# Kernel optimization log

Hardware: AMD Instinct MI355X
Metric: run time of the kernel (lower is better)

The kernel has to match this reference:

```python
import jax, jax.numpy as jnp
import numpy as np

POOL_NUM = 1024
NEIGHBOR_NUM = 16


def setup_inputs() -> dict:
    key = jax.random.key(0)
    k1, k2 = jax.random.split(key)
    vertices = jax.random.normal(k1, (8, 4096, 3), dtype=jnp.float32)
    feature_map = jax.random.normal(k2, (8, 4096, 256), dtype=jnp.float32)
    return {"vertices": vertices, "feature_map": feature_map}


def _get_neighbor_index(vertices, neighbor_num):
    # vertices: (bs, N, 3) -> neighbor_index: (bs, N, neighbor_num)
    inner = jnp.einsum('bnd,bmd->bnm', vertices, vertices)  # (bs, N, N)
    quadratic = jnp.sum(vertices ** 2, axis=2)              # (bs, N)
    distance = -2.0 * inner + quadratic[:, None, :] + quadratic[:, :, None]
    # smallest k+1 distances -> top_k on negated distance
    _, idx = jax.lax.top_k(-distance, neighbor_num + 1)     # (bs, N, k+1)
    return idx[:, :, 1:]                                    # drop self


def reference(vertices, feature_map):
    bs, vertice_num, _ = vertices.shape
    neighbor_index = _get_neighbor_index(vertices, NEIGHBOR_NUM)  # (bs, N, k)
    # gather neighbor features: (bs, N, k, C)
    id_0 = jnp.arange(bs)[:, None, None]
    neighbor_feature = feature_map[id_0, neighbor_index]
    pooled_feature = jnp.max(neighbor_feature, axis=2)            # (bs, N, C)
    # deterministic random subsample of vertices (torch uses randperm)
    sample_idx = jax.random.permutation(jax.random.key(42), vertice_num)[:POOL_NUM]
    vertices_pool = vertices[:, sample_idx, :]                    # (bs, P, 3)
    feature_map_pool = pooled_feature[:, sample_idx, :]           # (bs, P, C)
    return (vertices_pool, feature_map_pool)
```

## Files before the change

### kernel.cpp

```cpp
#include <hip/hip_runtime.h>
#include <stdint.h>
#include <string.h>
#include <algorithm>

#define NV 4096
#define NPOOL 1024
#define NB 8
#define KNB 16
#define REMOVED 0xFFFFFFFFu
#define HIDX(b) ((((b) >> 4) | (((b) & 15) << 6)))

struct SIdx { unsigned short v[NPOOL]; };

static inline void tf2x32_host(uint32_t k0, uint32_t k1,
                               uint32_t c0, uint32_t c1,
                               uint32_t& o0, uint32_t& o1) {
  uint32_t ks0 = k0, ks1 = k1, ks2 = k0 ^ k1 ^ 0x1BD11BDAu;
  uint32_t x0 = c0 + ks0, x1 = c1 + ks1;
#define TFR(r) { x0 += x1; x1 = (x1 << (r)) | (x1 >> (32 - (r))); x1 ^= x0; }
  TFR(13) TFR(15) TFR(26) TFR(6)
  x0 += ks1; x1 += ks2 + 1u;
  TFR(17) TFR(29) TFR(16) TFR(24)
  x0 += ks2; x1 += ks0 + 2u;
  TFR(13) TFR(15) TFR(26) TFR(6)
  x0 += ks0; x1 += ks1 + 3u;
  TFR(17) TFR(29) TFR(16) TFR(24)
  x0 += ks1; x1 += ks2 + 4u;
  TFR(13) TFR(15) TFR(26) TFR(6)
  x0 += ks2; x1 += ks0 + 5u;
#undef TFR
  o0 = x0; o1 = x1;
}

static void compute_sample_idx(SIdx& out) {
  static_assert(sizeof(SIdx) == 2048, "kernarg size");
  uint64_t arr[NV];
  uint16_t x[NV], tmp[NV];
  for (int i = 0; i < NV; ++i) x[i] = (uint16_t)i;
  uint32_t kh = 0u, kl = 42u;
  for (int round = 0; round < 2; ++round) {
    uint32_t nkh, nkl, sh, sl, t0, t1;
    tf2x32_host(kh, kl, 0u, 0u, nkh, nkl);
    tf2x32_host(kh, kl, 0u, 1u, sh, sl);
    kh = nkh; kl = nkl;
    for (int i = 0; i < NV; ++i) {
      tf2x32_host(sh, sl, 0u, (uint32_t)i, t0, t1);
      arr[i] = ((uint64_t)(t0 ^ t1) << 32) | (uint32_t)i;
    }
    std::sort(arr, arr + NV);
    for (int i = 0; i < NV; ++i) tmp[i] = x[(uint32_t)(arr[i] & 0xffffffffu)];
    memcpy(x, tmp, sizeof(x));
  }
  for (int i = 0; i < NPOOL; ++i) out.v[i] = x[i];
}

#define FALLBACK(D, TAUB, WIN)                                             \
  {                                                                        \
    uint32_t mask = 0;                                                     \
    for (int r = 0; r < KNB; ++r) {                                        \
      uint32_t bv = REMOVED, bm = 0xFFFFFFFFu;                             \
      _Pragma("unroll")                                                    \
      for (int t = 0; t < 16; ++t) {                                       \
        const uint32_t v = (((mask >> t) & 1u) || ((D[t] >> 22) > (TAUB))) \
                               ? REMOVED : D[t];                           \
        const uint32_t m = (uint32_t)((tid << 4) + t);                     \
        if (v < bv || (v == bv && m < bm)) { bv = v; bm = m; }             \
      }                                                                    \
      for (int off = 32; off > 0; off >>= 1) {                             \
        const uint32_t ov = (uint32_t)__shfl_down((int)bv, off);           \
        const uint32_t om = (uint32_t)__shfl_down((int)bm, off);           \
        if (ov < bv || (ov == bv && om < bm)) { bv = ov; bm = om; }        \
      }                                                                    \
      if (lane == 0) wmin[warp] = ((unsigned long long)bv << 32) | bm;     \
      __syncthreads();                                                     \
      const unsigned long long p0 = wmin[0], p1 = wmin[1];                 \
      const unsigned long long p2 = wmin[2], p3 = wmin[3];                 \
      const unsigned long long pa = (p0 < p1) ? p0 : p1;                   \
      const unsigned long long pb = (p2 < p3) ? p2 : p3;                   \
      const int w = (int)(((pa < pb) ? pa : pb) & 0xFFFFFFFFu);            \
      if (tid == 0) (WIN)[r] = w;                                          \
      if (tid == (w >> 4)) mask |= 1u << (w & 15);                         \
      __syncthreads();                                                     \
    }                                                                      \
  }

__global__ __launch_bounds__(256) void knn_pool_kernel(
    const float* __restrict__ vertices, const float* __restrict__ fm,
    const SIdx sidx,
    float* __restrict__ outV, float* __restrict__ outF) {
  __shared__ uint32_t hist0[1024], hist1[1024];
  __shared__ unsigned long long cand0[64], cand1[64];
  __shared__ unsigned long long wmin[4];
  __shared__ int winners0[KNB], winners1[KNB];
  __shared__ int s_nc0, s_nc1, s_tb0, s_tb1;

  const int tid = threadIdx.x;
  const int lane = tid & 63;
  const int warp = tid >> 6;
  const int blk = blockIdx.x;
  const int b = blk & 7;
  const int i0 = (blk >> 3) << 1;
  const int i1 = i0 | 1;
  const int n0 = (int)sidx.v[i0];
  const int n1 = (int)sidx.v[i1];

  const float* vb = vertices + (size_t)b * NV * 3;
  const float q0x = vb[n0 * 3 + 0], q0y = vb[n0 * 3 + 1], q0z = vb[n0 * 3 + 2];
  const float q1x = vb[n1 * 3 + 0], q1y = vb[n1 * 3 + 1], q1z = vb[n1 * 3 + 2];
  const float qn0 = __fadd_rn(__fadd_rn(__fmul_rn(q0x, q0x), __fmul_rn(q0y, q0y)),
                              __fmul_rn(q0z, q0z));
  const float qn1 = __fadd_rn(__fadd_rn(__fmul_rn(q1x, q1x), __fmul_rn(q1y, q1y)),
                              __fmul_rn(q1z, q1z));

  const float4* vb4 = (const float4*)vb + tid * 12;
  float f[48];
#pragma unroll
  for (int j = 0; j < 12; ++j) {
    const float4 v4 = vb4[j];
    f[4 * j + 0] = v4.x; f[4 * j + 1] = v4.y;
    f[4 * j + 2] = v4.z; f[4 * j + 3] = v4.w;
  }

  uint32_t d0[16], d1[16];
#pragma unroll
  for (int t = 0; t < 16; ++t) {
    const int m = (tid << 4) + t;
    const float cx = f[3 * t + 0], cy = f[3 * t + 1], cz = f[3 * t + 2];
    const float qm = __fadd_rn(__fadd_rn(__fmul_rn(cx, cx), __fmul_rn(cy, cy)),
                               __fmul_rn(cz, cz));
    const float in0 = __fmaf_rn(cz, q0z, __fmaf_rn(cy, q0y, __fmul_rn(cx, q0x)));
    const float in1 = __fmaf_rn(cz, q1z, __fmaf_rn(cy, q1y, __fmul_rn(cx, q1x)));
    const float ds0 = __fadd_rn(__fadd_rn(__fmul_rn(-2.0f, in0), qm), qn0);
    const float ds1 = __fadd_rn(__fadd_rn(__fmul_rn(-2.0f, in1), qm), qn1);
    d0[t] = (m == n0) ? REMOVED : __float_as_uint(ds0);
    d1[t] = (m == n1) ? REMOVED : __float_as_uint(ds1);
  }

  uint32_t mn0 = d0[0], mn1 = d1[0];
#pragma unroll
  for (int t = 1; t < 16; ++t) {
    mn0 = (d0[t] < mn0) ? d0[t] : mn0;
    mn1 = (d1[t] < mn1) ? d1[t] : mn1;
  }

  const uint4 z4 = make_uint4(0, 0, 0, 0);
  ((uint4*)hist0)[tid] = z4;
  ((uint4*)hist1)[tid] = z4;
  if (tid == 0) { s_nc0 = 0; s_nc1 = 0; }
  __syncthreads();

  atomicAdd(&hist0[HIDX(mn0 >> 22)], 1u);
  atomicAdd(&hist1[HIDX(mn1 >> 22)], 1u);
  __syncthreads();

  if (warp < 2) {
    uint32_t* H = (warp == 0) ? hist0 : hist1;
    uint32_t s = 0;
#pragma unroll
    for (int j = 0; j < 16; ++j) s += H[j * 64 + lane];
    uint32_t inc = s;
    for (int off = 1; off < 64; off <<= 1) {
      const uint32_t o = (uint32_t)__shfl_up((int)inc, off);
      if (lane >= off) inc += o;
    }
    const uint32_t pre = inc - s;
    const bool cross = (pre < KNB) && (inc >= KNB);
    const unsigned long long bal = __ballot(cross);
    const int leader = __ffsll((unsigned long long)bal) - 1;
    if (lane == leader) {
      uint32_t c = pre;
      int tb = lane * 16 + 15;
      for (int j = 0; j < 16; ++j) {
        const uint32_t h = H[j * 64 + lane];
        if (c + h >= KNB) { tb = lane * 16 + j; break; }
        c += h;
      }
      if (warp == 0) s_tb0 = tb; else s_tb1 = tb;
    }
  }
  __syncthreads();

  const uint32_t taub0 = (uint32_t)s_tb0;
  const uint32_t taub1 = (uint32_t)s_tb1;

#pragma unroll
  for (int t = 0; t < 16; ++t) {
    const uint32_t v0 = d0[t];
    if ((v0 >> 22) <= taub0) {
      const int s = atomicAdd(&s_nc0, 1);
      if (s < 64)
        cand0[s] = ((unsigned long long)v0 << 32) | (uint32_t)((tid << 4) + t);
    }
    const uint32_t v1 = d1[t];
    if ((v1 >> 22) <= taub1) {
      const int s = atomicAdd(&s_nc1, 1);
      if (s < 64)
        cand1[s] = ((unsigned long long)v1 << 32) | (uint32_t)((tid << 4) + t);
    }
  }
  __syncthreads();

  const int C0 = s_nc0, C1 = s_nc1;
  if (warp == 0 && C0 <= 64) {
    const unsigned long long me =
        (lane < C0) ? cand0[lane] : 0xFFFFFFFFFFFFFFFFull;
    int rank = 0;
    for (int j = 0; j < C0; ++j) rank += (cand0[j] < me) ? 1 : 0;
    if (lane < C0 && rank < KNB) winners0[rank] = (int)(me & 0xFFFFFFFFu);
  }
  if (warp == 1 && C1 <= 64) {
    const unsigned long long me =
        (lane < C1) ? cand1[lane] : 0xFFFFFFFFFFFFFFFFull;
    int rank = 0;
    for (int j = 0; j < C1; ++j) rank += (cand1[j] < me) ? 1 : 0;
    if (lane < C1 && rank < KNB) winners1[rank] = (int)(me & 0xFFFFFFFFu);
  }
  __syncthreads();

  if (C0 > 64) FALLBACK(d0, taub0, winners0);
  if (C1 > 64) FALLBACK(d1, taub1, winners1);

  const float* fmb = fm + (size_t)b * NV * 256;
  if (warp < 2) {
    const int* W = (warp == 0) ? winners0 : winners1;
    const int ii = (warp == 0) ? i0 : i1;
    float4 acc = make_float4(-INFINITY, -INFINITY, -INFINITY, -INFINITY);
#pragma unroll
    for (int s = 0; s < KNB; ++s) {
      const float4 v = ((const float4*)(fmb + (size_t)W[s] * 256))[lane];
      acc.x = fmaxf(acc.x, v.x); acc.y = fmaxf(acc.y, v.y);
      acc.z = fmaxf(acc.z, v.z); acc.w = fmaxf(acc.w, v.w);
    }
    ((float4*)(outF + ((size_t)b * NPOOL + ii) * 256))[lane] = acc;
  }
  if (warp == 2 && lane < 3) outV[((size_t)b * NPOOL + i0) * 3 + lane] = vb[n0 * 3 + lane];
  if (warp == 3 && lane < 3) outV[((size_t)b * NPOOL + i1) * 3 + lane] = vb[n1 * 3 + lane];
}

extern "C" void kernel_launch(void* const* d_in, const int* in_sizes, int n_in,
                              void* d_out, int out_size, void* d_ws, size_t ws_size,
                              hipStream_t stream) {
  const float* vertices = (const float*)d_in[0];
  const float* fm = (const float*)d_in[1];
  float* out = (float*)d_out;
  float* outV = out;
  float* outF = out + NB * NPOOL * 3;

  SIdx sidx;
  compute_sample_idx(sidx);

  knn_pool_kernel<<<NB * NPOOL / 2, 256, 0, stream>>>(vertices, fm, sidx, outV, outF);
}
```

Before: 36.11 us.

## Process four query points per block to amortize candidate vertex loads

```diff
diff --git a/kernel.cpp b/kernel.cpp
--- a/kernel.cpp
+++ b/kernel.cpp
@@ -84,33 +84,48 @@
     }                                                                      \
   }
 
+#define APPEND(D, TAUB, QI)                                                \
+  _Pragma("unroll")                                                        \
+  for (int t = 0; t < 16; ++t) {                                           \
+    const uint32_t v = D[t];                                               \
+    if ((v >> 22) <= (TAUB)) {                                             \
+      const int s = atomicAdd(&s_nc[QI], 1);                               \
+      if (s < 64)                                                          \
+        cand[QI][s] =                                                      \
+            ((unsigned long long)v << 32) | (uint32_t)((tid << 4) + t);    \
+    }                                                                      \
+  }
+
 __global__ __launch_bounds__(256) void knn_pool_kernel(
     const float* __restrict__ vertices, const float* __restrict__ fm,
     const SIdx sidx,
     float* __restrict__ outV, float* __restrict__ outF) {
-  __shared__ uint32_t hist0[1024], hist1[1024];
-  __shared__ unsigned long long cand0[64], cand1[64];
+  __shared__ uint32_t hist[4][1024];
+  __shared__ unsigned long long cand[4][64];
   __shared__ unsigned long long wmin[4];
-  __shared__ int winners0[KNB], winners1[KNB];
-  __shared__ int s_nc0, s_nc1, s_tb0, s_tb1;
+  __shared__ int winners[4][KNB];
+  __shared__ int s_nc[4], s_tb[4];
 
   const int tid = threadIdx.x;
   const int lane = tid & 63;
   const int warp = tid >> 6;
   const int blk = blockIdx.x;
   const int b = blk & 7;
-  const int i0 = (blk >> 3) << 1;
-  const int i1 = i0 | 1;
-  const int n0 = (int)sidx.v[i0];
-  const int n1 = (int)sidx.v[i1];
+  const int ibase = (blk >> 3) << 2;
+  const int n0 = (int)sidx.v[ibase + 0];
+  const int n1 = (int)sidx.v[ibase + 1];
+  const int n2 = (int)sidx.v[ibase + 2];
+  const int n3 = (int)sidx.v[ibase + 3];
 
   const float* vb = vertices + (size_t)b * NV * 3;
   const float q0x = vb[n0 * 3 + 0], q0y = vb[n0 * 3 + 1], q0z = vb[n0 * 3 + 2];
   const float q1x = vb[n1 * 3 + 0], q1y = vb[n1 * 3 + 1], q1z = vb[n1 * 3 + 2];
-  const float qn0 = __fadd_rn(__fadd_rn(__fmul_rn(q0x, q0x), __fmul_rn(q0y, q0y)),
-                              __fmul_rn(q0z, q0z));
-  const float qn1 = __fadd_rn(__fadd_rn(__fmul_rn(q1x, q1x), __fmul_rn(q1y, q1y)),
-                              __fmul_rn(q1z, q1z));
+  const float q2x = vb[n2 * 3 + 0], q2y = vb[n2 * 3 + 1], q2z = vb[n2 * 3 + 2];
+  const float q3x = vb[n3 * 3 + 0], q3y = vb[n3 * 3 + 1], q3z = vb[n3 * 3 + 2];
+  const float qn0 = __fadd_rn(__fadd_rn(__fmul_rn(q0x, q0x), __fmul_rn(q0y, q0y)), __fmul_rn(q0z, q0z));
+  const float qn1 = __fadd_rn(__fadd_rn(__fmul_rn(q1x, q1x), __fmul_rn(q1y, q1y)), __fmul_rn(q1z, q1z));
+  const float qn2 = __fadd_rn(__fadd_rn(__fmul_rn(q2x, q2x), __fmul_rn(q2y, q2y)), __fmul_rn(q2z, q2z));
+  const float qn3 = __fadd_rn(__fadd_rn(__fmul_rn(q3x, q3x), __fmul_rn(q3y, q3y)), __fmul_rn(q3z, q3z));
 
   const float4* vb4 = (const float4*)vb + tid * 12;
   float f[48];
@@ -121,7 +136,7 @@
     f[4 * j + 2] = v4.z; f[4 * j + 3] = v4.w;
   }
 
-  uint32_t d0[16], d1[16];
+  uint32_t d0[16], d1[16], d2[16], d3[16];
 #pragma unroll
   for (int t = 0; t < 16; ++t) {
     const int m = (tid << 4) + t;
@@ -130,31 +145,43 @@
                                __fmul_rn(cz, cz));
     const float in0 = __fmaf_rn(cz, q0z, __fmaf_rn(cy, q0y, __fmul_rn(cx, q0x)));
     const float in1 = __fmaf_rn(cz, q1z, __fmaf_rn(cy, q1y, __fmul_rn(cx, q1x)));
+    const float in2 = __fmaf_rn(cz, q2z, __fmaf_rn(cy, q2y, __fmul_rn(cx, q2x)));
+    const float in3 = __fmaf_rn(cz, q3z, __fmaf_rn(cy, q3y, __fmul_rn(cx, q3x)));
     const float ds0 = __fadd_rn(__fadd_rn(__fmul_rn(-2.0f, in0), qm), qn0);
     const float ds1 = __fadd_rn(__fadd_rn(__fmul_rn(-2.0f, in1), qm), qn1);
+    const float ds2 = __fadd_rn(__fadd_rn(__fmul_rn(-2.0f, in2), qm), qn2);
+    const float ds3 = __fadd_rn(__fadd_rn(__fmul_rn(-2.0f, in3), qm), qn3);
     d0[t] = (m == n0) ? REMOVED : __float_as_uint(ds0);
     d1[t] = (m == n1) ? REMOVED : __float_as_uint(ds1);
-  }
-
-  uint32_t mn0 = d0[0], mn1 = d1[0];
+    d2[t] = (m == n2) ? REMOVED : __float_as_uint(ds2);
+    d3[t] = (m == n3) ? REMOVED : __float_as_uint(ds3);
+  }
+
+  uint32_t mn0 = d0[0], mn1 = d1[0], mn2 = d2[0], mn3 = d3[0];
 #pragma unroll
   for (int t = 1; t < 16; ++t) {
     mn0 = (d0[t] < mn0) ? d0[t] : mn0;
     mn1 = (d1[t] < mn1) ? d1[t] : mn1;
-  }
-
-  const uint4 z4 = make_uint4(0, 0, 0, 0);
-  ((uint4*)hist0)[tid] = z4;
-  ((uint4*)hist1)[tid] = z4;
-  if (tid == 0) { s_nc0 = 0; s_nc1 = 0; }
-  __syncthreads();
-
-  atomicAdd(&hist0[HIDX(mn0 >> 22)], 1u);
-  atomicAdd(&hist1[HIDX(mn1 >> 22)], 1u);
-  __syncthreads();
-
-  if (warp < 2) {
-    uint32_t* H = (warp == 0) ? hist0 : hist1;
+    mn2 = (d2[t] < mn2) ? d2[t] : mn2;
+    mn3 = (d3[t] < mn3) ? d3[t] : mn3;
+  }
+
+  {
+    const uint4 z4 = make_uint4(0, 0, 0, 0);
+    uint4* h4 = (uint4*)&hist[0][0];
+    h4[tid] = z4; h4[tid + 256] = z4; h4[tid + 512] = z4; h4[tid + 768] = z4;
+  }
+  if (tid < 4) s_nc[tid] = 0;
+  __syncthreads();
+
+  atomicAdd(&hist[0][HIDX(mn0 >> 22)], 1u);
+  atomicAdd(&hist[1][HIDX(mn1 >> 22)], 1u);
+  atomicAdd(&hist[2][HIDX(mn2 >> 22)], 1u);
+  atomicAdd(&hist[3][HIDX(mn3 >> 22)], 1u);
+  __syncthreads();
+
+  {
+    const uint32_t* H = hist[warp];
     uint32_t s = 0;
 #pragma unroll
     for (int j = 0; j < 16; ++j) s += H[j * 64 + lane];
@@ -175,55 +202,44 @@
         if (c + h >= KNB) { tb = lane * 16 + j; break; }
         c += h;
       }
-      if (warp == 0) s_tb0 = tb; else s_tb1 = tb;
-    }
-  }
-  __syncthreads();
-
-  const uint32_t taub0 = (uint32_t)s_tb0;
-  const uint32_t taub1 = (uint32_t)s_tb1;
-
-#pragma unroll
-  for (int t = 0; t < 16; ++t) {
-    const uint32_t v0 = d0[t];
-    if ((v0 >> 22) <= taub0) {
-      const int s = atomicAdd(&s_nc0, 1);
-      if (s < 64)
-        cand0[s] = ((unsigned long long)v0 << 32) | (uint32_t)((tid << 4) + t);
-    }
-    const uint32_t v1 = d1[t];
-    if ((v1 >> 22) <= taub1) {
-      const int s = atomicAdd(&s_nc1, 1);
-      if (s < 64)
-        cand1[s] = ((unsigned long long)v1 << 32) | (uint32_t)((tid << 4) + t);
-    }
-  }
-  __syncthreads();
-
-  const int C0 = s_nc0, C1 = s_nc1;
-  if (warp == 0 && C0 <= 64) {
-    const unsigned long long me =
-        (lane < C0) ? cand0[lane] : 0xFFFFFFFFFFFFFFFFull;
-    int rank = 0;
-    for (int j = 0; j < C0; ++j) rank += (cand0[j] < me) ? 1 : 0;
-    if (lane < C0 && rank < KNB) winners0[rank] = (int)(me & 0xFFFFFFFFu);
-  }
-  if (warp == 1 && C1 <= 64) {
-    const unsigned long long me =
-        (lane < C1) ? cand1[lane] : 0xFFFFFFFFFFFFFFFFull;
-    int rank = 0;
-    for (int j = 0; j < C1; ++j) rank += (cand1[j] < me) ? 1 : 0;
-    if (lane < C1 && rank < KNB) winners1[rank] = (int)(me & 0xFFFFFFFFu);
-  }
-  __syncthreads();
-
-  if (C0 > 64) FALLBACK(d0, taub0, winners0);
-  if (C1 > 64) FALLBACK(d1, taub1, winners1);
+      s_tb[warp] = tb;
+    }
+  }
+  __syncthreads();
+
+  const uint32_t taub0 = (uint32_t)s_tb[0];
+  const uint32_t taub1 = (uint32_t)s_tb[1];
+  const uint32_t taub2 = (uint32_t)s_tb[2];
+  const uint32_t taub3 = (uint32_t)s_tb[3];
+
+  APPEND(d0, taub0, 0)
+  APPEND(d1, taub1, 1)
+  APPEND(d2, taub2, 2)
+  APPEND(d3, taub3, 3)
+  __syncthreads();
+
+  const int C0 = s_nc[0], C1 = s_nc[1], C2 = s_nc[2], C3 = s_nc[3];
+  {
+    const int C = s_nc[warp];
+    if (C <= 64) {
+      const unsigned long long me =
+          (lane < C) ? cand[warp][lane] : 0xFFFFFFFFFFFFFFFFull;
+      int rank = 0;
+      for (int j = 0; j < C; ++j) rank += (cand[warp][j] < me) ? 1 : 0;
+      if (lane < C && rank < KNB) winners[warp][rank] = (int)(me & 0xFFFFFFFFu);
+    }
+  }
+  __syncthreads();
+
+  if (C0 > 64) FALLBACK(d0, taub0, winners[0]);
+  if (C1 > 64) FALLBACK(d1, taub1, winners[1]);
+  if (C2 > 64) FALLBACK(d2, taub2, winners[2]);
+  if (C3 > 64) FALLBACK(d3, taub3, winners[3]);
 
   const float* fmb = fm + (size_t)b * NV * 256;
-  if (warp < 2) {
-    const int* W = (warp == 0) ? winners0 : winners1;
-    const int ii = (warp == 0) ? i0 : i1;
+  {
+    const int* W = winners[warp];
+    const int ii = ibase + warp;
     float4 acc = make_float4(-INFINITY, -INFINITY, -INFINITY, -INFINITY);
 #pragma unroll
     for (int s = 0; s < KNB; ++s) {
@@ -232,9 +248,11 @@
       acc.z = fmaxf(acc.z, v.z); acc.w = fmaxf(acc.w, v.w);
     }
     ((float4*)(outF + ((size_t)b * NPOOL + ii) * 256))[lane] = acc;
-  }
-  if (warp == 2 && lane < 3) outV[((size_t)b * NPOOL + i0) * 3 + lane] = vb[n0 * 3 + lane];
-  if (warp == 3 && lane < 3) outV[((size_t)b * NPOOL + i1) * 3 + lane] = vb[n1 * 3 + lane];
+    if (lane < 3) {
+      const int nn = (warp == 0) ? n0 : (warp == 1) ? n1 : (warp == 2) ? n2 : n3;
+      outV[((size_t)b * NPOOL + ii) * 3 + lane] = vb[nn * 3 + lane];
+    }
+  }
 }
 
 extern "C" void kernel_launch(void* const* d_in, const int* in_sizes, int n_in,
@@ -249,5 +267,5 @@
   SIdx sidx;
   compute_sample_idx(sidx);
 
-  knn_pool_kernel<<<NB * NPOOL / 2, 256, 0, stream>>>(vertices, fm, sidx, outV, outF);
-}
+  knn_pool_kernel<<<NB * NPOOL / 4, 256, 0, stream>>>(vertices, fm, sidx, outV, outF);
+}
```

Result: slower. 42.84 us (+18.6%).
